# Kernel optimization log

Hardware: AMD Instinct MI355X
Metric: run time of the kernel (lower is better)

The kernel has to match this reference:

```python
import jax, jax.numpy as jnp
import numpy as np

ALPHA = 0.01  # ema_decay

def setup_inputs() -> dict:
    key = jax.random.key(0)
    k1, k2 = jax.random.split(key)
    B, S, H = 8, 2048, 2048
    x = jax.random.normal(k1, (B, S, H), dtype=jnp.float32)
    W = jax.random.normal(k2, (H, H), dtype=jnp.float32) * (1.0 / np.sqrt(H))
    b = jnp.zeros((H,), dtype=jnp.float32)
    return {"x": x, "W": W, "b": b}

def reference(x, W, b):
    B, S, H = x.shape
    dt = x.dtype
    # p = [S-1, S-2, ..., 0]; w_prime = (1-alpha)^p
    p = jnp.arange(S - 1, -1, -1, dtype=dt)
    one_m_a = jnp.asarray(1.0 - ALPHA, dtype=dt)
    w_prime = one_m_a ** p                                   # [S]
    # w = w_prime, but positions t>=1 scaled by alpha
    w = jnp.where(jnp.arange(S) >= 1, w_prime * ALPHA, w_prime)  # [S]
    c = jnp.cumsum(x * w[None, :, None], axis=1)             # [B,S,H]
    s = c / w_prime[None, :, None]                           # [B,S,H]
    # nn.Linear: s @ W^T + b
    return jnp.einsum('bsh,oh->bso', s, W) + b
```

## Files before the change

kernel.cpp:

```cpp
#include <hip/hip_runtime.h>
#include <cstdint>
#include <cstddef>

#define ALPHA 0.01f
#define A1    0.99f
#define B_    8
#define S_    2048
#define H_    2048
#define NCH   8
#define CL    256
#define NKT   32

typedef __attribute__((ext_vector_type(8))) short bf16x8;
typedef __attribute__((ext_vector_type(4))) float f32x4;

__device__ __forceinline__ unsigned short f2bf(float f) {
    unsigned int u = __float_as_uint(f);
    u += 0x7FFFu + ((u >> 16) & 1u);
    return (unsigned short)(u >> 16);
}

__device__ __forceinline__ void gld16(const void* g, void* l) {
    __builtin_amdgcn_global_load_lds(
        (const __attribute__((address_space(1))) unsigned int*)g,
        (__attribute__((address_space(3))) unsigned int*)l, 16, 0, 0);
}

__global__ void ema_cast_w(const float* __restrict__ W, short* __restrict__ Wb) {
    int i = (blockIdx.x * 256 + threadIdx.x) * 4;
    float4 v = *(const float4*)(W + i);
    short4 o;
    o.x = (short)f2bf(v.x);
    o.y = (short)f2bf(v.y);
    o.z = (short)f2bf(v.z);
    o.w = (short)f2bf(v.w);
    *(short4*)(Wb + i) = o;
}

__global__ __launch_bounds__(256) void ema_carry_kernel(
        const float* __restrict__ x, float* __restrict__ carry) {
    int bid = blockIdx.x;
    int hg = bid & 3;
    int c  = (bid >> 2) & 7;
    int b  = bid >> 5;
    int h0 = (hg << 9) + (threadIdx.x << 1);
    const float2* px = (const float2*)(x + ((size_t)(b * S_) + (size_t)c * CL) * H_ + h0);
    const int STR = H_ / 2;
    float s0, s1;
    int i0;
    if (c == 0) { float2 v = px[0]; s0 = v.x; s1 = v.y; i0 = 1; }
    else        { s0 = 0.f; s1 = 0.f;                   i0 = 0; }
    #pragma unroll 8
    for (int i = i0; i < CL; ++i) {
        float2 v = px[(size_t)i * STR];
        s0 = fmaf(A1, s0, ALPHA * v.x);
        s1 = fmaf(A1, s1, ALPHA * v.y);
    }
    *(float2*)(carry + ((b << 3) + c) * H_ + h0) = (float2){s0, s1};
}

__global__ __launch_bounds__(256) void ema_apply_kernel(
        const float* __restrict__ x, const float* __restrict__ carry,
        unsigned short* __restrict__ sb) {
    int bid = blockIdx.x;
    int hg = bid & 3;
    int c  = (bid >> 2) & 7;
    int b  = bid >> 5;
    int h0 = (hg << 9) + (threadIdx.x << 1);

    float A256 = A1;
    #pragma unroll
    for (int q = 0; q < 8; ++q) A256 *= A256;

    float c0 = 0.f, c1 = 0.f, f = 1.f;
    for (int j = c - 1; j >= 0; --j) {
        float2 cv = *(const float2*)(carry + ((b << 3) + j) * H_ + h0);
        c0 = fmaf(cv.x, f, c0);
        c1 = fmaf(cv.y, f, c1);
        f *= A256;
    }

    size_t base = ((size_t)(b * S_) + (size_t)c * CL) * H_ + h0;
    const float2* px = (const float2*)(x + base);
    unsigned int*  pu = (unsigned int*)(sb + base);
    const int STR = H_ / 2;
    float s0, s1;
    int i0;
    if (c == 0) {
        float2 v = px[0]; s0 = v.x; s1 = v.y;
        pu[0] = (unsigned int)f2bf(s0) | ((unsigned int)f2bf(s1) << 16);
        i0 = 1;
    } else { s0 = c0; s1 = c1; i0 = 0; }
    #pragma unroll 8
    for (int i = i0; i < CL; ++i) {
        float2 v = px[(size_t)i * STR];
        s0 = fmaf(A1, s0, ALPHA * v.x);
        s1 = fmaf(A1, s1, ALPHA * v.y);
        pu[(size_t)i * STR] = (unsigned int)f2bf(s0) | ((unsigned int)f2bf(s1) << 16);
    }
}


#define BAR __builtin_amdgcn_s_barrier()
#define WAIT_LGKM do { asm volatile("s_waitcnt lgkmcnt(0)" ::: "memory"); \
                       __builtin_amdgcn_sched_barrier(0); } while (0)
#define VMW(n) asm volatile("s_waitcnt vmcnt(" #n ")" ::: "memory")

#define STGA(i, kt, buf) gld16(gA[i] + (size_t)(kt) * 128, &ldsA[buf][((i) << 12) + (w << 9)])
#define STGB(i, kt, buf) gld16(gB[i] + (size_t)(kt) * 128, &ldsB[buf][((i) << 12) + (w << 9)])

#define LDA(mh) do { int ra_ = (wm << 1) | (mh);                                   \
    const char* base_ = (const char*)&ldsA[cur][0]                                 \
        + (((((ra_ & 1) << 1) | (ra_ >> 1))) << 13) + laneRow;                     \
    _Pragma("unroll") for (int m_ = 0; m_ < 4; ++m_) {                             \
        Af[m_][0] = *(const bf16x8*)(base_ + (m_ << 11) + ck0);                    \
        Af[m_][1] = *(const bf16x8*)(base_ + (m_ << 11) + ck1); } } while (0)

#define LDB(nh) do { const char* base_ = (const char*)&ldsB[cur][0]                \
        + ((nh) << 14) + (wn << 12) + laneRow;                                     \
    _Pragma("unroll") for (int n_ = 0; n_ < 2; ++n_) {                             \
        Bf[(nh) * 2 + n_][0] = *(const bf16x8*)(base_ + (n_ << 11) + ck0);         \
        Bf[(nh) * 2 + n_][1] = *(const bf16x8*)(base_ + (n_ << 11) + ck1); } } while (0)

#define MM(mh, nh) do { __builtin_amdgcn_s_setprio(1);                             \
    _Pragma("unroll") for (int m_ = 0; m_ < 4; ++m_)                               \
    _Pragma("unroll") for (int n_ = 0; n_ < 2; ++n_)                               \
    _Pragma("unroll") for (int k_ = 0; k_ < 2; ++k_)                               \
        acc[(mh) * 4 + m_][(nh) * 2 + n_] = __builtin_amdgcn_mfma_f32_16x16x32_bf16( \
            Af[m_][k_], Bf[(nh) * 2 + n_][k_], acc[(mh) * 4 + m_][(nh) * 2 + n_], 0, 0, 0); \
    __builtin_amdgcn_s_setprio(0); } while (0)

__global__ __launch_bounds__(512, 2) void ema_gemm_kernel(
        const short* __restrict__ Sb, const short* __restrict__ Wb,
        const float* __restrict__ bias, float* __restrict__ out) {
    __shared__ short ldsA[2][16384];
    __shared__ short ldsB[2][16384];

    int bid = blockIdx.x;
    int swz = ((bid & 7) << 6) | (bid >> 3);
    int tm = swz >> 3;
    int tn = swz & 7;

    int tid  = threadIdx.x;
    int lane = tid & 63;
    int w    = tid >> 6;
    int wm   = w >> 2;
    int wn   = w & 3;

    const int K2 = H_ * 2;
    int rowA = tm << 8;
    int rowB = tn << 8;

    int rowoff = (w << 3) + (lane >> 3);
    int colb   = (((lane & 7) ^ (lane >> 3)) << 4);
    const char* SbB = (const char*)Sb;
    const char* WbB = (const char*)Wb;
    const char* gA[4];
    const char* gB[4];
    #pragma unroll
    for (int i = 0; i < 4; ++i) {
        int lq = ((i & 1) << 1) | (i >> 1);
        gA[i] = SbB + (size_t)(rowA + lq * 64 + rowoff) * K2 + colb;
        int pos = 2 * i + (w >> 2);
        int ls  = ((pos & 3) << 1) | (pos >> 2);
        gB[i] = WbB + (size_t)(rowB + ls * 32 + ((w & 3) << 3) + (lane >> 3)) * K2 + colb;
    }

    int laneRow = (lane & 15) << 7;
    int ck0 = (((lane >> 4)) ^ (lane & 7)) << 4;
    int ck1 = ((4 + (lane >> 4)) ^ (lane & 7)) << 4;

    f32x4 acc[8][4];
    #pragma unroll
    for (int i = 0; i < 8; ++i)
        #pragma unroll
        for (int j = 0; j < 4; ++j)
            acc[i][j] = (f32x4){0.f, 0.f, 0.f, 0.f};
    bf16x8 Af[4][2], Bf[4][2];

    int colg = (tn << 8) + (wn << 6) + (lane & 15);
    float bb[4];
    #pragma unroll
    for (int n = 0; n < 4; ++n) bb[n] = bias[colg + (n << 4)];

    STGA(0, 0, 0); STGA(1, 0, 0); STGB(0, 0, 0); STGB(1, 0, 0);
    STGA(2, 0, 0); STGA(3, 0, 0); STGB(2, 0, 0); STGB(3, 0, 0);
    STGA(0, 1, 1); STGA(1, 1, 1); STGB(0, 1, 1); STGB(1, 1, 1);
    VMW(6);
    BAR;

    for (int t = 0; t < NKT; ++t) {
        int cur = t & 1, nxt = cur ^ 1;
        bool i01 = (t < NKT - 1), i23 = (t < NKT - 2);
        LDA(0); LDB(0);
        if (i01) { STGA(2, t + 1, nxt); STGA(3, t + 1, nxt); }
        BAR; WAIT_LGKM;
        MM(0, 0);
        if (i01) { VMW(6); }
        BAR;
        LDB(1);
        if (i01) { STGB(2, t + 1, nxt); STGB(3, t + 1, nxt); }
        BAR; WAIT_LGKM;
        MM(0, 1);
        BAR;
        LDA(1);
        if (i23) { STGA(0, t + 2, cur); STGA(1, t + 2, cur); }
        BAR; WAIT_LGKM;
        MM(1, 0);
        BAR;
        if (i23) { STGB(0, t + 2, cur); STGB(1, t + 2, cur); }
        BAR;
        MM(1, 1);
        if (t == NKT - 2) { VMW(0); }
        else if (t < NKT - 2) { VMW(6); }
        BAR;
    }

    int rowg = (tm << 8) + (wm << 7) + ((lane >> 4) << 2);
    #pragma unroll
    for (int m = 0; m < 8; ++m) {
        #pragma unroll
        for (int n = 0; n < 4; ++n) {
            int c = colg + (n << 4);
            size_t rb = (size_t)(rowg + (m << 4)) << 11;
            #pragma unroll
            for (int q = 0; q < 4; ++q)
                out[rb + ((size_t)q << 11) + c] = acc[m][n][q] + bb[n];
        }
    }
}

extern "C" void kernel_launch(void* const* d_in, const int* in_sizes, int n_in,
                              void* d_out, int out_size, void* d_ws, size_t ws_size,
                              hipStream_t stream) {
    const float* x    = (const float*)d_in[0];
    const float* W    = (const float*)d_in[1];
    const float* bias = (const float*)d_in[2];
    float* out = (float*)d_out;

    char* ws = (char*)d_ws;
    size_t s_bytes = (size_t)B_ * S_ * H_ * 2;
    size_t w_bytes = (size_t)H_ * H_ * 2;
    unsigned short* s_bf  = (unsigned short*)ws;
    short*          w_bf  = (short*)(ws + s_bytes);
    float*          carry = (float*)(ws + s_bytes + w_bytes);

    ema_cast_w<<<(H_ * H_) / 1024, 256, 0, stream>>>(W, w_bf);
    ema_carry_kernel<<<B_ * NCH * (H_ / 512), 256, 0, stream>>>(x, carry);
    ema_apply_kernel<<<B_ * NCH * (H_ / 512), 256, 0, stream>>>(x, carry, s_bf);
    ema_gemm_kernel<<<(16384 / 256) * (2048 / 256), 512, 0, stream>>>(
        (const short*)s_bf, w_bf, bias, out);
}
```

Measured before the change: 192.0 us.

## Restructure GEMM main loop to load whole k-tile into registers and prefetch two ahead

The main loop now reads all A and B fragments for a k-tile from LDS up front into separate register sets (Af0/Af1), then issues the MFMAs with only two barriers per iteration instead of eight. Global-to-LDS staging of the full next-next tile is issued in one batch between the two MFMA halves, and the prologue preloads two full tiles. This cuts barrier and waitcnt overhead and lets LDS reads overlap MFMA work. In exchange it uses more registers, which may pressure the two-blocks-per-CU occupancy, and the coarser staging may expose more global latency.

```diff
diff --git a/kernel.cpp b/kernel.cpp
--- a/kernel.cpp
+++ b/kernel.cpp
@@ -109,12 +109,12 @@
 #define STGA(i, kt, buf) gld16(gA[i] + (size_t)(kt) * 128, &ldsA[buf][((i) << 12) + (w << 9)])
 #define STGB(i, kt, buf) gld16(gB[i] + (size_t)(kt) * 128, &ldsB[buf][((i) << 12) + (w << 9)])
 
-#define LDA(mh) do { int ra_ = (wm << 1) | (mh);                                   \
+#define LDAm(dst, mh) do { int ra_ = (wm << 1) | (mh);                             \
     const char* base_ = (const char*)&ldsA[cur][0]                                 \
         + (((((ra_ & 1) << 1) | (ra_ >> 1))) << 13) + laneRow;                     \
     _Pragma("unroll") for (int m_ = 0; m_ < 4; ++m_) {                             \
-        Af[m_][0] = *(const bf16x8*)(base_ + (m_ << 11) + ck0);                    \
-        Af[m_][1] = *(const bf16x8*)(base_ + (m_ << 11) + ck1); } } while (0)
+        dst[m_][0] = *(const bf16x8*)(base_ + (m_ << 11) + ck0);                   \
+        dst[m_][1] = *(const bf16x8*)(base_ + (m_ << 11) + ck1); } } while (0)
 
 #define LDB(nh) do { const char* base_ = (const char*)&ldsB[cur][0]                \
         + ((nh) << 14) + (wn << 12) + laneRow;                                     \
@@ -122,12 +122,12 @@
         Bf[(nh) * 2 + n_][0] = *(const bf16x8*)(base_ + (n_ << 11) + ck0);         \
         Bf[(nh) * 2 + n_][1] = *(const bf16x8*)(base_ + (n_ << 11) + ck1); } } while (0)
 
-#define MM(mh, nh) do { __builtin_amdgcn_s_setprio(1);                             \
+#define MMq(Asrc, mh, nh) do { __builtin_amdgcn_s_setprio(1);                      \
     _Pragma("unroll") for (int m_ = 0; m_ < 4; ++m_)                               \
     _Pragma("unroll") for (int n_ = 0; n_ < 2; ++n_)                               \
     _Pragma("unroll") for (int k_ = 0; k_ < 2; ++k_)                               \
         acc[(mh) * 4 + m_][(nh) * 2 + n_] = __builtin_amdgcn_mfma_f32_16x16x32_bf16( \
-            Af[m_][k_], Bf[(nh) * 2 + n_][k_], acc[(mh) * 4 + m_][(nh) * 2 + n_], 0, 0, 0); \
+            Asrc[m_][k_], Bf[(nh) * 2 + n_][k_], acc[(mh) * 4 + m_][(nh) * 2 + n_], 0, 0, 0); \
     __builtin_amdgcn_s_setprio(0); } while (0)
 
 __global__ __launch_bounds__(512, 2) void ema_gemm_kernel(
@@ -176,43 +176,37 @@
         #pragma unroll
         for (int j = 0; j < 4; ++j)
             acc[i][j] = (f32x4){0.f, 0.f, 0.f, 0.f};
-    bf16x8 Af[4][2], Bf[4][2];
+    bf16x8 Af0[4][2], Af1[4][2], Bf[4][2];
 
     int colg = (tn << 8) + (wn << 6) + (lane & 15);
     float bb[4];
     #pragma unroll
     for (int n = 0; n < 4; ++n) bb[n] = bias[colg + (n << 4)];
 
-    STGA(0, 0, 0); STGA(1, 0, 0); STGB(0, 0, 0); STGB(1, 0, 0);
-    STGA(2, 0, 0); STGA(3, 0, 0); STGB(2, 0, 0); STGB(3, 0, 0);
-    STGA(0, 1, 1); STGA(1, 1, 1); STGB(0, 1, 1); STGB(1, 1, 1);
-    VMW(6);
+    STGA(0, 0, 0); STGA(1, 0, 0); STGA(2, 0, 0); STGA(3, 0, 0);
+    STGB(0, 0, 0); STGB(1, 0, 0); STGB(2, 0, 0); STGB(3, 0, 0);
+    STGA(0, 1, 1); STGA(1, 1, 1); STGA(2, 1, 1); STGA(3, 1, 1);
+    STGB(0, 1, 1); STGB(1, 1, 1); STGB(2, 1, 1); STGB(3, 1, 1);
+    VMW(8);
     BAR;
 
     for (int t = 0; t < NKT; ++t) {
-        int cur = t & 1, nxt = cur ^ 1;
-        bool i01 = (t < NKT - 1), i23 = (t < NKT - 2);
-        LDA(0); LDB(0);
-        if (i01) { STGA(2, t + 1, nxt); STGA(3, t + 1, nxt); }
-        BAR; WAIT_LGKM;
-        MM(0, 0);
-        if (i01) { VMW(6); }
+        int cur = t & 1;
+        LDAm(Af0, 0); LDB(0); LDB(1); LDAm(Af1, 1);
+        MMq(Af0, 0, 0);
+        MMq(Af0, 0, 1);
+        WAIT_LGKM;
         BAR;
-        LDB(1);
-        if (i01) { STGB(2, t + 1, nxt); STGB(3, t + 1, nxt); }
-        BAR; WAIT_LGKM;
-        MM(0, 1);
-        BAR;
-        LDA(1);
-        if (i23) { STGA(0, t + 2, cur); STGA(1, t + 2, cur); }
-        BAR; WAIT_LGKM;
-        MM(1, 0);
-        BAR;
-        if (i23) { STGB(0, t + 2, cur); STGB(1, t + 2, cur); }
-        BAR;
-        MM(1, 1);
-        if (t == NKT - 2) { VMW(0); }
-        else if (t < NKT - 2) { VMW(6); }
+        if (t < NKT - 2) {
+            STGA(0, t + 2, cur); STGA(1, t + 2, cur);
+            STGA(2, t + 2, cur); STGA(3, t + 2, cur);
+            STGB(0, t + 2, cur); STGB(1, t + 2, cur);
+            STGB(2, t + 2, cur); STGB(3, t + 2, cur);
+        }
+        MMq(Af1, 1, 0);
+        MMq(Af1, 1, 1);
+        if (t < NKT - 2)       { VMW(8); }
+        else if (t == NKT - 2) { VMW(0); }
         BAR;
     }
 
```

Result: slower. 204.9 us (+6.7%).
